# Performance work log

Hardware: AMD Instinct MI355X
Metric: run time of the kernel (lower is better)

The kernel has to match this reference:

```python
import jax, jax.numpy as jnp
import numpy as np

B, T = 64, 2048
D_RNN, D_EMB, D_ATT = 1024, 512, 128
N_FILT, KSIZE = 32, 31
PAD = (KSIZE - 1) // 2


def setup_inputs() -> dict:
    key = jax.random.key(0)
    ks = jax.random.split(key, 9)
    return {
        "attention_hidden_state": jax.random.normal(ks[0], (B, D_RNN), jnp.float32),
        "memory": jax.random.normal(ks[1], (B, T, D_EMB), jnp.float32),
        "processed_memory": jax.random.normal(ks[2], (B, T, D_ATT), jnp.float32),
        "attention_weights_cat": jax.random.uniform(ks[3], (B, 2, T), jnp.float32),
        "mask": jax.random.randint(ks[4], (B, T), 0, 2) > 0,
        # learned params (all bias-free, as in the torch module)
        "Wq": jax.random.normal(ks[5], (D_ATT, D_RNN), jnp.float32) * 0.02,   # query_layer.weight
        "Wv": jax.random.normal(ks[6], (1, D_ATT), jnp.float32) * 0.02,        # v.weight
        "conv_w": jax.random.normal(ks[7], (N_FILT, 2, KSIZE), jnp.float32) * 0.1,  # location_conv.weight (OIH)
        "Wd": jax.random.normal(ks[8], (D_ATT, N_FILT), jnp.float32) * 0.02,   # location_dense.weight
    }


def reference(attention_hidden_state, memory, processed_memory,
              attention_weights_cat, mask, Wq, Wv, conv_w, Wd):
    # processed query: [B, 1, D_ATT]
    pq = (attention_hidden_state @ Wq.T)[:, None, :]
    # location features: Conv1d(2 -> N_FILT, same padding) over time
    loc = jax.lax.conv_general_dilated(
        attention_weights_cat, conv_w,
        window_strides=(1,), padding=[(PAD, PAD)],
        dimension_numbers=("NCH", "OIH", "NCH"))           # [B, N_FILT, T]
    paw = jnp.einsum("bft,af->bta", loc, Wd)               # [B, T, D_ATT]
    # additive energies -> scalar per position via v-projection
    energies = jnp.einsum("bta,a->bt", jnp.tanh(pq + paw + processed_memory), Wv[0])
    alignment = jnp.where(mask, -jnp.inf, energies)         # masked fill
    attention_weights = jax.nn.softmax(alignment, axis=1)   # [B, T]
    attention_context = jnp.einsum("bt,btd->bd", attention_weights, memory)  # [B, D_EMB]
    return attention_context, jax.lax.stop_gradient(attention_weights)
```

## Files before the change

### kernel.cpp

```cpp
#include <hip/hip_runtime.h>
#include <math.h>

#define B_    64
#define T_    2048
#define DRNN  1024
#define DEMB  512
#define DATT  128
#define NF    32
#define KS    31
#define PADL  15
#define MP    64
#define TT    32
#define CT    64
#define NC    (T_/CT)

__device__ __forceinline__ float fast_tanh(float x){
    float e2 = __expf(2.0f * x);
    return 1.0f - 2.0f / (e2 + 1.0f);
}

__global__ __launch_bounds__(128) void prep_kernel(
    const float* __restrict__ hidden, const float* __restrict__ Wq,
    const float* __restrict__ Wd, const float* __restrict__ convw,
    float* __restrict__ pq, float* __restrict__ M)
{
    const int blk = blockIdx.x;
    const int a = threadIdx.x;
    if (blk < B_) {
        __shared__ float sh[DRNN];
        const int b = blk;
        #pragma unroll
        for (int i = 0; i < DRNN/128; ++i) sh[a + 128*i] = hidden[b*DRNN + a + 128*i];
        __syncthreads();
        const float4* wq4 = (const float4*)(Wq + a*DRNN);
        float acc = 0.f;
        #pragma unroll 4
        for (int k = 0; k < DRNN/4; ++k){
            float4 w = wq4[k];
            acc = fmaf(w.x, sh[4*k+0], acc);
            acc = fmaf(w.y, sh[4*k+1], acc);
            acc = fmaf(w.z, sh[4*k+2], acc);
            acc = fmaf(w.w, sh[4*k+3], acc);
        }
        pq[b*DATT + a] = acc;
    } else {
        float wd[NF];
        #pragma unroll
        for (int f = 0; f < NF; ++f) wd[f] = Wd[a*NF + f];
        for (int ck = 0; ck < 2*KS; ++ck){
            float acc = 0.f;
            #pragma unroll
            for (int f = 0; f < NF; ++f) acc = fmaf(wd[f], convw[f*2*KS + ck], acc);
            M[a*MP + ck] = acc;
        }
    }
}

__global__ __launch_bounds__(256) void fused_kernel(
    const float* __restrict__ pm, const float* __restrict__ awcat,
    const float* __restrict__ pq, const float* __restrict__ M,
    const float* __restrict__ Wv, const int* __restrict__ mask,
    const float* __restrict__ memory,
    float* __restrict__ pbuf, float* __restrict__ pmax,
    float* __restrict__ psum, float* __restrict__ pctx)
{
    const int b   = blockIdx.y;
    const int cx  = blockIdx.x;
    const int t0  = cx * CT;
    const int tid = threadIdx.x;
    const int s   = tid >> 7;
    const int a   = tid & 127;
    const int ts  = t0 + TT * s;

    __shared__ float saw0[96], saw1[96];
    __shared__ float sred[2][2][TT];
    __shared__ float2 swt[CT];
    __shared__ int   scount;
    __shared__ float4 sacc[128];

    for (int i = tid; i < 94; i += 256){
        int tt = t0 - PADL + i;
        bool ok = (tt >= 0) && (tt < T_);
        saw0[i] = ok ? awcat[(b*2+0)*T_ + tt] : 0.f;
        saw1[i] = ok ? awcat[(b*2+1)*T_ + tt] : 0.f;
    }
    __syncthreads();

    float Ma0[KS], Ma1[KS];
    const float* Mrow = M + a*MP;
    #pragma unroll
    for (int k = 0; k < KS; ++k){ Ma0[k] = Mrow[k]; Ma1[k] = Mrow[KS + k]; }
    const float pqa = pq[b*DATT + a];
    const float wv  = Wv[a];

    float acc[TT];
    #pragma unroll
    for (int t = 0; t < TT; ++t) acc[t] = pqa;

    #pragma unroll
    for (int j = 0; j < TT + KS - 1; ++j){
        const float av0 = saw0[j + TT*s];
        const float av1 = saw1[j + TT*s];
        const int tlo = (j - KS + 1) > 0 ? (j - KS + 1) : 0;
        const int thi = (j < TT - 1) ? j : (TT - 1);
        #pragma unroll
        for (int t = tlo; t <= thi; ++t){
            acc[t] = fmaf(Ma0[j - t], av0, acc[t]);
            acc[t] = fmaf(Ma1[j - t], av1, acc[t]);
        }
    }

    const float* pmb = pm + ((size_t)(b*T_ + ts)) * DATT + a;
    #pragma unroll
    for (int t = 0; t < TT; ++t){
        float x = acc[t] + pmb[(size_t)t * DATT];
        acc[t] = wv * fast_tanh(x);
    }

    const int lane = tid & 63;
    const int half = a >> 6;
    #pragma unroll
    for (int t = 0; t < TT; ++t){
        float r = acc[t];
        r += __shfl_xor(r, 1, 64);  r += __shfl_xor(r, 2, 64);
        r += __shfl_xor(r, 4, 64);  r += __shfl_xor(r, 8, 64);
        r += __shfl_xor(r, 16, 64); r += __shfl_xor(r, 32, 64);
        if (lane == 0) sred[s][half][t] = r;
    }
    __syncthreads();

    if (tid < 64){
        const int t = t0 + tid;
        float e = sred[tid>>5][0][tid&31] + sred[tid>>5][1][tid&31];
        const int mk = mask[b*T_ + t];
        float mval = mk ? -1e30f : e;
        #pragma unroll
        for (int off = 1; off < 64; off <<= 1) mval = fmaxf(mval, __shfl_xor(mval, off, 64));
        const float pval = mk ? 0.f : __expf(e - mval);
        float sv = pval;
        #pragma unroll
        for (int off = 1; off < 64; off <<= 1) sv += __shfl_xor(sv, off, 64);
        pbuf[b*T_ + t] = pval;
        const unsigned long long bal = __ballot(pval != 0.f);
        if (pval != 0.f){
            const int pfx = (int)__popcll(bal & ((1ull << tid) - 1ull));
            swt[pfx] = make_float2(pval, __int_as_float(tid));
        }
        if (tid == 0){
            scount = (int)__popcll(bal);
            pmax[b*NC + cx] = mval;
            psum[b*NC + cx] = sv;
        }
    }
    __syncthreads();

    const int n   = scount;
    const int col = tid & 127;
    const int row = tid >> 7;
    float4 a4 = make_float4(0.f, 0.f, 0.f, 0.f);
    const float4* mem4 = (const float4*)memory + ((size_t)(b*T_ + t0))*(DEMB/4) + col;

    int i = row;
    for (; i + 6 < n; i += 8){
        const float2 e0 = swt[i];
        const float2 e1 = swt[i+2];
        const float2 e2 = swt[i+4];
        const float2 e3 = swt[i+6];
        const float4 m0 = mem4[(size_t)__float_as_int(e0.y) * (DEMB/4)];
        const float4 m1 = mem4[(size_t)__float_as_int(e1.y) * (DEMB/4)];
        const float4 m2 = mem4[(size_t)__float_as_int(e2.y) * (DEMB/4)];
        const float4 m3 = mem4[(size_t)__float_as_int(e3.y) * (DEMB/4)];
        a4.x = fmaf(e0.x, m0.x, a4.x); a4.y = fmaf(e0.x, m0.y, a4.y);
        a4.z = fmaf(e0.x, m0.z, a4.z); a4.w = fmaf(e0.x, m0.w, a4.w);
        a4.x = fmaf(e1.x, m1.x, a4.x); a4.y = fmaf(e1.x, m1.y, a4.y);
        a4.z = fmaf(e1.x, m1.z, a4.z); a4.w = fmaf(e1.x, m1.w, a4.w);
        a4.x = fmaf(e2.x, m2.x, a4.x); a4.y = fmaf(e2.x, m2.y, a4.y);
        a4.z = fmaf(e2.x, m2.z, a4.z); a4.w = fmaf(e2.x, m2.w, a4.w);
        a4.x = fmaf(e3.x, m3.x, a4.x); a4.y = fmaf(e3.x, m3.y, a4.y);
        a4.z = fmaf(e3.x, m3.z, a4.z); a4.w = fmaf(e3.x, m3.w, a4.w);
    }
    for (; i < n; i += 2){
        const float2 e = swt[i];
        const float4 m = mem4[(size_t)__float_as_int(e.y) * (DEMB/4)];
        a4.x = fmaf(e.x, m.x, a4.x); a4.y = fmaf(e.x, m.y, a4.y);
        a4.z = fmaf(e.x, m.z, a4.z); a4.w = fmaf(e.x, m.w, a4.w);
    }

    if (row == 1) sacc[col] = a4;
    __syncthreads();
    if (row == 0){
        const float4 o = sacc[col];
        float4* dst = (float4*)(pctx + ((size_t)(b*NC + cx))*DEMB) + col;
        *dst = make_float4(a4.x + o.x, a4.y + o.y, a4.z + o.z, a4.w + o.w);
    }
}

__global__ __launch_bounds__(256) void finalize_kernel(
    const float* __restrict__ pbuf, const float* __restrict__ pmax,
    const float* __restrict__ psum, const float* __restrict__ pctx,
    float* __restrict__ ctx, float* __restrict__ wout)
{
    const int b = blockIdx.x;
    const int tid = threadIdx.x;
    __shared__ float sscale[NC];

    if (tid < 64){
        float mv = (tid < NC) ? pmax[b*NC + tid] : -1e30f;
        float sv = (tid < NC) ? psum[b*NC + tid] : 0.f;
        float g = mv;
        #pragma unroll
        for (int off = 1; off < 64; off <<= 1) g = fmaxf(g, __shfl_xor(g, off, 64));
        float z = sv * __expf(mv - g);
        #pragma unroll
        for (int off = 1; off < 64; off <<= 1) z += __shfl_xor(z, off, 64);
        if (tid < NC) sscale[tid] = __expf(mv - g) / z;
    }
    __syncthreads();

    float2 a2 = make_float2(0.f, 0.f);
    const float2* pc2 = (const float2*)(pctx + (size_t)b*NC*DEMB) + tid;
    #pragma unroll
    for (int c = 0; c < NC; ++c){
        const float sc = sscale[c];
        if (sc != 0.f){
            const float2 v = pc2[(size_t)c * (DEMB/2)];
            a2.x = fmaf(sc, v.x, a2.x);
            a2.y = fmaf(sc, v.y, a2.y);
        }
    }
    ((float2*)(ctx + b*DEMB))[tid] = a2;

    #pragma unroll
    for (int i = 0; i < T_/256; ++i){
        const int t = tid + 256*i;
        wout[b*T_ + t] = pbuf[b*T_ + t] * sscale[t >> 6];
    }
}

extern "C" void kernel_launch(void* const* d_in, const int* in_sizes, int n_in,
                              void* d_out, int out_size, void* d_ws, size_t ws_size,
                              hipStream_t stream)
{
    const float* hidden = (const float*)d_in[0];
    const float* memory = (const float*)d_in[1];
    const float* pm     = (const float*)d_in[2];
    const float* awcat  = (const float*)d_in[3];
    const int*   mask   = (const int*)d_in[4];
    const float* Wq     = (const float*)d_in[5];
    const float* Wv     = (const float*)d_in[6];
    const float* convw  = (const float*)d_in[7];
    const float* Wd     = (const float*)d_in[8];

    float* out  = (float*)d_out;
    float* ctx  = out;
    float* wout = out + B_*DEMB;

    float* pq    = (float*)d_ws;
    float* M     = pq   + B_*DATT;
    float* pbuf  = M    + DATT*MP;
    float* pmax  = pbuf + B_*T_;
    float* psum  = pmax + B_*NC;
    float* pctx  = psum + B_*NC;

    prep_kernel<<<dim3(B_ + 1), 128, 0, stream>>>(hidden, Wq, Wd, convw, pq, M);
    fused_kernel<<<dim3(NC, B_), 256, 0, stream>>>(pm, awcat, pq, M, Wv, mask,
                                                   memory, pbuf, pmax, psum, pctx);
    finalize_kernel<<<dim3(B_), 256, 0, stream>>>(pbuf, pmax, psum, pctx, ctx, wout);
}
```

Baseline: 456.8 us.

## Use transpose-style butterfly reduction across time rows and prefetch processed memory early

Result: faster. 441.2 us (-3.4%).

```diff
diff --git a/kernel.cpp b/kernel.cpp
--- a/kernel.cpp
+++ b/kernel.cpp
@@ -86,16 +86,18 @@
     }
     __syncthreads();
 
+    const float pqa = pq[b*DATT + a];
+    const float wv  = Wv[a];
+    const float* pmb = pm + ((size_t)(b*T_ + ts)) * DATT + a;
+
+    float acc[TT];
+    #pragma unroll
+    for (int t = 0; t < TT; ++t) acc[t] = pqa + pmb[(size_t)t * DATT];
+
     float Ma0[KS], Ma1[KS];
     const float* Mrow = M + a*MP;
     #pragma unroll
     for (int k = 0; k < KS; ++k){ Ma0[k] = Mrow[k]; Ma1[k] = Mrow[KS + k]; }
-    const float pqa = pq[b*DATT + a];
-    const float wv  = Wv[a];
-
-    float acc[TT];
-    #pragma unroll
-    for (int t = 0; t < TT; ++t) acc[t] = pqa;
 
     #pragma unroll
     for (int j = 0; j < TT + KS - 1; ++j){
@@ -110,23 +112,52 @@
         }
     }
 
-    const float* pmb = pm + ((size_t)(b*T_ + ts)) * DATT + a;
     #pragma unroll
     for (int t = 0; t < TT; ++t){
-        float x = acc[t] + pmb[(size_t)t * DATT];
-        acc[t] = wv * fast_tanh(x);
+        acc[t] = wv * fast_tanh(acc[t]);
     }
 
     const int lane = tid & 63;
     const int half = a >> 6;
     #pragma unroll
-    for (int t = 0; t < TT; ++t){
-        float r = acc[t];
-        r += __shfl_xor(r, 1, 64);  r += __shfl_xor(r, 2, 64);
-        r += __shfl_xor(r, 4, 64);  r += __shfl_xor(r, 8, 64);
-        r += __shfl_xor(r, 16, 64); r += __shfl_xor(r, 32, 64);
-        if (lane == 0) sred[s][half][t] = r;
-    }
+    for (int k = 0; k < 16; ++k){
+        const bool hi = (lane & 1) != 0;
+        float send = hi ? acc[k] : acc[k+16];
+        float recv = __shfl_xor(send, 1, 64);
+        acc[k] = (hi ? acc[k+16] : acc[k]) + recv;
+    }
+    #pragma unroll
+    for (int k = 0; k < 8; ++k){
+        const bool hi = (lane & 2) != 0;
+        float send = hi ? acc[k] : acc[k+8];
+        float recv = __shfl_xor(send, 2, 64);
+        acc[k] = (hi ? acc[k+8] : acc[k]) + recv;
+    }
+    #pragma unroll
+    for (int k = 0; k < 4; ++k){
+        const bool hi = (lane & 4) != 0;
+        float send = hi ? acc[k] : acc[k+4];
+        float recv = __shfl_xor(send, 4, 64);
+        acc[k] = (hi ? acc[k+4] : acc[k]) + recv;
+    }
+    #pragma unroll
+    for (int k = 0; k < 2; ++k){
+        const bool hi = (lane & 8) != 0;
+        float send = hi ? acc[k] : acc[k+2];
+        float recv = __shfl_xor(send, 8, 64);
+        acc[k] = (hi ? acc[k+2] : acc[k]) + recv;
+    }
+    {
+        const bool hi = (lane & 16) != 0;
+        float send = hi ? acc[0] : acc[1];
+        float recv = __shfl_xor(send, 16, 64);
+        acc[0] = (hi ? acc[1] : acc[0]) + recv;
+    }
+    acc[0] += __shfl_xor(acc[0], 32, 64);
+    const int trev = ((lane & 1) << 4) | (((lane >> 1) & 1) << 3) |
+                     (((lane >> 2) & 1) << 2) | (((lane >> 3) & 1) << 1) |
+                     ((lane >> 4) & 1);
+    if (lane < 32) sred[s][half][trev] = acc[0];
     __syncthreads();
 
     if (tid < 64){
```
